# Kernel tuning notes

Hardware: AMD Instinct MI355X
Metric: run time of the kernel (lower is better)

## Reference

```python
import jax, jax.numpy as jnp
import numpy as np

N_FFT = 512; HOP = 256; WIN = 512
FDRC = 0.5; ORDER = 5; SPKS = 2
NFREQ = N_FFT // 2 + 1           # 257
HID = 512
PROJ = 2 * ORDER * SPKS * NFREQ  # 5140
LN_EPS = 1e-5
_WINDOW = 0.5 - 0.5 * jnp.cos(2 * jnp.pi * jnp.arange(WIN) / WIN)  # periodic hann


def _stft(x):
    # x: [B, L] -> complex spec [B, F, T], center-padded (reflect), hann window
    pad = N_FFT // 2
    xp = jnp.pad(x, ((0, 0), (pad, pad)), mode='reflect')
    T = 1 + (xp.shape[1] - N_FFT) // HOP
    idx = jnp.arange(T)[:, None] * HOP + jnp.arange(N_FFT)[None, :]
    frames = xp[:, idx] * _WINDOW            # [B, T, n_fft]
    spec = jnp.fft.rfft(frames, axis=-1)     # [B, T, F]
    return spec.transpose(0, 2, 1)           # [B, F, T]


def _istft(spec, length):
    # spec: [B, F, T] complex -> waveform [B, length] via overlap-add with window-square norm
    pad = N_FFT // 2
    frames = jnp.fft.irfft(spec.transpose(0, 2, 1), n=N_FFT, axis=-1) * _WINDOW  # [B,T,n_fft]
    B, T, _ = frames.shape
    total = length + 2 * pad
    idx = (jnp.arange(T)[:, None] * HOP + jnp.arange(N_FFT)[None, :]).ravel()
    out = jnp.zeros((B, total), frames.dtype).at[:, idx].add(frames.reshape(B, -1))
    wsq = jnp.zeros((total,), frames.dtype).at[idx].add(jnp.tile(_WINDOW ** 2, T))
    seg = wsq[pad:pad + length]
    return out[:, pad:pad + length] / jnp.where(seg > 1e-11, seg, 1.0)


def _lstm(xs, W_ih, W_hh, b_ih, b_hh):
    # xs: [T, B, in]; torch gate order i,f,g,o; returns hidden sequence [T, B, H]
    T, B, _ = xs.shape
    H = W_hh.shape[1]
    xs_proj = xs @ W_ih.T + (b_ih + b_hh)    # hoist input projection out of scan

    def step(carry, xp_t):
        h, c = carry
        gates = xp_t + h @ W_hh.T
        i, f, g, o = jnp.split(gates, 4, axis=-1)
        c = jax.nn.sigmoid(f) * c + jax.nn.sigmoid(i) * jnp.tanh(g)
        h = jax.nn.sigmoid(o) * jnp.tanh(c)
        return (h, c), h

    init = (jnp.zeros((B, H), xs.dtype), jnp.zeros((B, H), xs.dtype))
    _, hs = jax.lax.scan(step, init, xs_proj)
    return hs


def setup_inputs() -> dict:
    key = jax.random.key(0)
    ks = jax.random.split(key, 14)
    s = 0.04  # ~ 1/sqrt(hidden)
    return {
        'x': jax.random.normal(ks[0], (32, 160000), dtype=jnp.float32),
        'ln_g': jnp.ones((NFREQ,), jnp.float32),
        'ln_b': jnp.zeros((NFREQ,), jnp.float32),
        'W_ih0': jax.random.normal(ks[1], (4 * HID, NFREQ), jnp.float32) * s,
        'W_hh0': jax.random.normal(ks[2], (4 * HID, HID), jnp.float32) * s,
        'b_ih0': jax.random.normal(ks[3], (4 * HID,), jnp.float32) * s,
        'b_hh0': jax.random.normal(ks[4], (4 * HID,), jnp.float32) * s,
        'W_ih1': jax.random.normal(ks[5], (4 * HID, HID), jnp.float32) * s,
        'W_hh1': jax.random.normal(ks[6], (4 * HID, HID), jnp.float32) * s,
        'b_ih1': jax.random.normal(ks[7], (4 * HID,), jnp.float32) * s,
        'b_hh1': jax.random.normal(ks[8], (4 * HID,), jnp.float32) * s,
        'proj_W': jax.random.normal(ks[9], (PROJ, HID), jnp.float32) * s,
        'proj_b': jax.random.normal(ks[10], (PROJ,), jnp.float32) * s,
    }


def reference(x, ln_g, ln_b, W_ih0, W_hh0, b_ih0, b_hh0,
              W_ih1, W_hh1, b_ih1, b_hh1, proj_W, proj_b):
    B, L = x.shape
    spec = _stft(x)                      # [B, F, T] complex
    T = spec.shape[-1]
    mag = jnp.abs(spec) ** FDRC          # [B, F, T]

    # full-band sequence model (pre-LN -> 2-layer LSTM -> proj -> tanh)
    h = mag.transpose(2, 0, 1)           # [T, B, F]
    mu = h.mean(-1, keepdims=True)
    var = h.var(-1, keepdims=True)
    h = (h - mu) / jnp.sqrt(var + LN_EPS) * ln_g + ln_b
    h = _lstm(h, W_ih0, W_hh0, b_ih0, b_hh0)
    h = _lstm(h, W_ih1, W_hh1, b_ih1, b_hh1)
    h = jnp.tanh(h @ proj_W.T + proj_b)  # [T, B, 2*d*s*F]
    fb = h.transpose(1, 2, 0)            # [B, 2*d*s*F, T]

    # deep-filter coefficients: 'b (c d s f) t -> b d s f t c' -> complex [B,d,s,F,T]
    coef = fb.reshape(B, 2, ORDER, SPKS, NFREQ, T)
    coef_c = jax.lax.complex(coef[:, 0], coef[:, 1])

    # unfold spectrogram along time with left pad of (order-1): [B, F, T, d]
    padded = jnp.pad(spec, ((0, 0), (0, 0), (ORDER - 1, 0)))
    spec_unf = jnp.stack([padded[:, :, d:d + T] for d in range(ORDER)], axis=-1)

    # out[b,s,f,t] = sum_d spec_unf[b,f,t,d] * coef[b,d,s,f,t]
    enh = jnp.einsum('bftd,bdsft->bsft', spec_unf, coef_c)  # [B, S, F, T]

    enh_y = _istft(enh.reshape(B * SPKS, NFREQ, T), L).reshape(B, SPKS, L)
    return enh_y
```

## Files before the change

### kernel.cpp

```cpp
#include <hip/hip_runtime.h>
#include <hip/hip_cooperative_groups.h>
#include <math.h>

#define BATCH 32
#define LEN   160000
#define NFFT  512
#define NT    626
#define NF    257
#define NFP   288
#define HID   512
#define PROJN 5140
#define TC    32
#define NCHUNK 20
#define K0    800
#define K1    1024
#define NLSTM 64
#define NWORK 192
#define NBLKT 256

typedef unsigned short ushort;
typedef __attribute__((ext_vector_type(8))) short short8;
typedef __attribute__((ext_vector_type(4))) float f32x4;

__device__ __forceinline__ float sigm(float x){ return 1.0f/(1.0f+expf(-x)); }
__device__ __forceinline__ ushort f2bf(float f){
  union{float f;unsigned u;} v; v.f=f;
  unsigned r = v.u + 0x7fffu + ((v.u>>16)&1u);
  return (ushort)(r>>16);
}

__global__ __launch_bounds__(256) void k_init(float* tw, int* zr, int nz){
  int i = blockIdx.x*256 + threadIdx.x;
  if (i < 512){
    float ang = 6.28318530717958647692f * (float)i / 512.0f;
    tw[i]     = cosf(ang);
    tw[512+i] = sinf(ang);
  }
  for (int j = i; j < nz; j += gridDim.x*256) zr[j] = 0;
}

__global__ __launch_bounds__(256) void k_zero(float* p, int n){
  for (int i = blockIdx.x*256 + threadIdx.x; i < n; i += gridDim.x*256) p[i] = 0.f;
}

__global__ __launch_bounds__(256) void k_prep(const float* __restrict__ Wih0, const float* __restrict__ Whh0,
                                              const float* __restrict__ bih0, const float* __restrict__ bhh0,
                                              const float* __restrict__ Wih1, const float* __restrict__ Whh1,
                                              const float* __restrict__ bih1, const float* __restrict__ bhh1,
                                              const float* __restrict__ projW,
                                              ushort* __restrict__ W0, ushort* __restrict__ W1,
                                              float* __restrict__ b0c, float* __restrict__ b1c,
                                              ushort* __restrict__ projWb){
  const int n0 = 2048*K0, n1 = 2048*K1, n2 = PROJN*HID;
  for (int i = blockIdx.x*256 + threadIdx.x; i < n0 + n1 + 4096 + n2; i += gridDim.x*256){
    if (i < n0){
      int r = i / K0, c = i - r*K0;
      float v = (c < 257) ? Wih0[(size_t)r*257 + c] : (c < NFP ? 0.f : Whh0[(size_t)r*512 + (c-NFP)]);
      W0[i] = f2bf(v);
    } else if (i < n0 + n1){
      int j = i - n0;
      int r = j / K1, c = j - r*K1;
      float v = (c < 512) ? Wih1[(size_t)r*512 + c] : Whh1[(size_t)r*512 + (c-512)];
      W1[j] = f2bf(v);
    } else if (i < n0 + n1 + 4096){
      int j = i - n0 - n1;
      if (j < 2048) b0c[j] = bih0[j] + bhh0[j];
      else          b1c[j-2048] = bih1[j-2048] + bhh1[j-2048];
    } else {
      int j = i - n0 - n1 - 4096;
      projWb[j] = f2bf(projW[j]);
    }
  }
}

__global__ __launch_bounds__(256) void k_stftln(const float* __restrict__ x, const float* __restrict__ tw,
                                                const float* __restrict__ g, const float* __restrict__ be,
                                                ushort* __restrict__ hlnb){
  int b = blockIdx.x / NT;
  int t = blockIdx.x % NT;
  __shared__ float fr[NFFT], mg[NF];
  __shared__ float red[16];
  const float* xb = x + (size_t)b*LEN;
  for (int n = threadIdx.x; n < NFFT; n += 256){
    int j = t*256 + n - 256;
    if (j < 0) j = -j;
    else if (j >= LEN) j = 2*LEN - 2 - j;
    fr[n] = xb[j] * (0.5f - 0.5f*tw[n]);
  }
  __syncthreads();
  float v=0.f, v2=0.f;
  for (int f = threadIdx.x; f < NF; f += 256){
    float c4 = tw[(4*f)&511], s4 = tw[512+((4*f)&511)];
    float cr0=1.f,            si0=0.f;
    float cr1=tw[f&511],      si1=tw[512+(f&511)];
    float cr2=tw[(2*f)&511],  si2=tw[512+((2*f)&511)];
    float cr3=tw[(3*f)&511],  si3=tw[512+((3*f)&511)];
    float ar0=0.f,ai0=0.f,ar1=0.f,ai1=0.f,ar2=0.f,ai2=0.f,ar3=0.f,ai3=0.f;
    #pragma unroll 4
    for (int n = 0; n < NFFT; n += 4){
      ar0 += fr[n  ]*cr0; ai0 -= fr[n  ]*si0;
      ar1 += fr[n+1]*cr1; ai1 -= fr[n+1]*si1;
      ar2 += fr[n+2]*cr2; ai2 -= fr[n+2]*si2;
      ar3 += fr[n+3]*cr3; ai3 -= fr[n+3]*si3;
      float tc, ts;
      tc = cr0*c4 - si0*s4; ts = cr0*s4 + si0*c4; cr0=tc; si0=ts;
      tc = cr1*c4 - si1*s4; ts = cr1*s4 + si1*c4; cr1=tc; si1=ts;
      tc = cr2*c4 - si2*s4; ts = cr2*s4 + si2*c4; cr2=tc; si2=ts;
      tc = cr3*c4 - si3*s4; ts = cr3*s4 + si3*c4; cr3=tc; si3=ts;
    }
    float ar = (ar0+ar1)+(ar2+ar3);
    float ai = (ai0+ai1)+(ai2+ai3);
    float m = sqrtf(sqrtf(ar*ar + ai*ai));
    mg[f]=m; v+=m; v2+=m*m;
  }
  for (int off=32; off; off>>=1){ v += __shfl_down(v,off); v2 += __shfl_down(v2,off); }
  int w = threadIdx.x >> 6;
  if ((threadIdx.x & 63)==0){ red[w]=v; red[8+w]=v2; }
  __syncthreads();
  if (threadIdx.x==0){
    float s  = red[0]+red[1]+red[2]+red[3];
    float s2 = red[8]+red[9]+red[10]+red[11];
    float mu = s/(float)NF;
    red[4]=mu;
    red[5]=rsqrtf(s2/(float)NF - mu*mu + 1e-5f);
  }
  __syncthreads();
  float mu=red[4], rs=red[5];
  size_t ob = ((size_t)t*BATCH + b)*NFP;
  for (int f=threadIdx.x; f<NFP; f+=256){
    float val = 0.f;
    if (f < NF) val = (mg[f]-mu)*rs*g[f] + be[f];
    hlnb[ob+f] = f2bf(val);
  }
}

__device__ void dev_stft_frame(const float* __restrict__ x, const float* __restrict__ tw,
                               float* __restrict__ spR, float* __restrict__ spI,
                               int tb0, int tt, int b, float* fr){
  int t = tb0 + tt;
  int tid = threadIdx.x;
  if (t < 0 || t >= NT){
    for (int f = tid; f < NF; f += 256){
      size_t o = ((size_t)b*NF + f)*36 + tt;
      spR[o]=0.f; spI[o]=0.f;
    }
    return;
  }
  const float* xb = x + (size_t)b*LEN;
  for (int n = tid; n < NFFT; n += 256){
    int j = t*256 + n - 256;
    if (j < 0) j = -j;
    else if (j >= LEN) j = 2*LEN - 2 - j;
    fr[n] = xb[j] * (0.5f - 0.5f*tw[n]);
  }
  __syncthreads();
  for (int f = tid; f < NF; f += 256){
    float c4 = tw[(4*f)&511], s4 = tw[512+((4*f)&511)];
    float cr0=1.f,            si0=0.f;
    float cr1=tw[f&511],      si1=tw[512+(f&511)];
    float cr2=tw[(2*f)&511],  si2=tw[512+((2*f)&511)];
    float cr3=tw[(3*f)&511],  si3=tw[512+((3*f)&511)];
    float ar0=0.f,ai0=0.f,ar1=0.f,ai1=0.f,ar2=0.f,ai2=0.f,ar3=0.f,ai3=0.f;
    #pragma unroll 4
    for (int n = 0; n < NFFT; n += 4){
      ar0 += fr[n  ]*cr0; ai0 -= fr[n  ]*si0;
      ar1 += fr[n+1]*cr1; ai1 -= fr[n+1]*si1;
      ar2 += fr[n+2]*cr2; ai2 -= fr[n+2]*si2;
      ar3 += fr[n+3]*cr3; ai3 -= fr[n+3]*si3;
      float tc, ts;
      tc = cr0*c4 - si0*s4; ts = cr0*s4 + si0*c4; cr0=tc; si0=ts;
      tc = cr1*c4 - si1*s4; ts = cr1*s4 + si1*c4; cr1=tc; si1=ts;
      tc = cr2*c4 - si2*s4; ts = cr2*s4 + si2*c4; cr2=tc; si2=ts;
      tc = cr3*c4 - si3*s4; ts = cr3*s4 + si3*c4; cr3=tc; si3=ts;
    }
    size_t o = ((size_t)b*NF + f)*36 + tt;
    spR[o] = (ar0+ar1)+(ar2+ar3);
    spI[o] = (ai0+ai1)+(ai2+ai3);
  }
  __syncthreads();
}

__device__ void dev_gemm_tile(const ushort* __restrict__ A, const ushort* __restrict__ Bb,
                              const float* __restrict__ bias, float* __restrict__ C,
                              int M, int N, int bx, int by){
  int bm = by*64, bn = bx*64;
  int wave = threadIdx.x >> 6, lane = threadIdx.x & 63;
  int wm = wave >> 1, wn = wave & 1;
  int col = lane & 15, kg = lane >> 4;
  f32x4 acc00={0.f,0.f,0.f,0.f}, acc01=acc00, acc10=acc00, acc11=acc00;
  const ushort* Ap = A + (size_t)(bm + wm*32)*512;
  int nr0 = bn + wn*32 + col;
  int nr1 = nr0 + 16;
  const ushort* Bp0 = Bb + (size_t)((nr0<N)?nr0:0)*512;
  const ushort* Bp1 = Bb + (size_t)((nr1<N)?nr1:0)*512;
  #pragma unroll 4
  for (int k0=0; k0<512; k0+=32){
    short8 a0 = *(const short8*)(Ap + (size_t)col*512 + k0 + kg*8);
    short8 a1 = *(const short8*)(Ap + (size_t)(16+col)*512 + k0 + kg*8);
    short8 b0 = *(const short8*)(Bp0 + k0 + kg*8);
    short8 b1 = *(const short8*)(Bp1 + k0 + kg*8);
    acc00 = __builtin_amdgcn_mfma_f32_16x16x32_bf16(a0, b0, acc00, 0, 0, 0);
    acc01 = __builtin_amdgcn_mfma_f32_16x16x32_bf16(a0, b1, acc01, 0, 0, 0);
    acc10 = __builtin_amdgcn_mfma_f32_16x16x32_bf16(a1, b0, acc10, 0, 0, 0);
    acc11 = __builtin_amdgcn_mfma_f32_16x16x32_bf16(a1, b1, acc11, 0, 0, 0);
  }
  #define STORE_ACC(ACC, MI, NI) { \
    int n = bn + wn*32 + (NI)*16 + col; \
    if (n < N){ \
      float bv = bias[n]; \
      _Pragma("unroll") \
      for (int j=0;j<4;j++){ \
        int m = bm + wm*32 + (MI)*16 + kg*4 + j; \
        C[(size_t)m*N + n] = tanhf(ACC[j] + bv); \
      } \
    } }
  STORE_ACC(acc00, 0, 0)
  STORE_ACC(acc01, 0, 1)
  STORE_ACC(acc10, 1, 0)
  STORE_ACC(acc11, 1, 1)
  #undef STORE_ACC
}

__device__ void dev_ifused_task(const float* __restrict__ prch,
    const float* __restrict__ spR, const float* __restrict__ spI,
    const float* __restrict__ tw, float* __restrict__ out, int tb0, int task,
    float* reb, float* imb){
  int tl = task >> 6;
  int b  = (task >> 1) & 31;
  int s  = task & 1;
  int tau = tb0 + 4 + tl;
  int tid = threadIdx.x;
  const float* p = prch + ((size_t)tl*BATCH + b)*PROJN;
  for (int f=tid; f<NF; f+=256){
    float ar=0.f, ai=0.f;
    size_t so = ((size_t)b*NF + f)*36;
    #pragma unroll
    for (int d=0; d<5; d++){
      int ts = tb0 + tl + d;
      if (ts >= 0){
        float sr=spR[so + tl + d], si=spI[so + tl + d];
        float cr=p[d*514 + s*257 + f];
        float ci=p[2570 + d*514 + s*257 + f];
        ar += sr*cr - si*ci;
        ai += sr*ci + si*cr;
      }
    }
    reb[f]=ar; imb[f]=ai;
  }
  __syncthreads();
  float* ob = out + (size_t)(b*2+s)*LEN;
  for (int n=tid; n<NFFT; n+=256){
    float c4 = tw[(4*n)&511], s4 = tw[512+((4*n)&511)];
    float crA=tw[n&511],     siA=tw[512+(n&511)];
    float crB=tw[(2*n)&511], siB=tw[512+((2*n)&511)];
    float crC=tw[(3*n)&511], siC=tw[512+((3*n)&511)];
    float crD=c4,            siD=s4;
    float a0=0.f,a1=0.f,a2=0.f,a3=0.f;
    #pragma unroll 4
    for (int m=0; m<63; m++){
      int k = 4*m+1;
      a0 += reb[k  ]*crA - imb[k  ]*siA;
      a1 += reb[k+1]*crB - imb[k+1]*siB;
      a2 += reb[k+2]*crC - imb[k+2]*siC;
      a3 += reb[k+3]*crD - imb[k+3]*siD;
      float tc, ts;
      tc = crA*c4 - siA*s4; ts = crA*s4 + siA*c4; crA=tc; siA=ts;
      tc = crB*c4 - siB*s4; ts = crB*s4 + siB*c4; crB=tc; siB=ts;
      tc = crC*c4 - siC*s4; ts = crC*s4 + siC*c4; crC=tc; siC=ts;
      tc = crD*c4 - siD*s4; ts = crD*s4 + siD*c4; crD=tc; siD=ts;
    }
    a0 += reb[253]*crA - imb[253]*siA;
    a1 += reb[254]*crB - imb[254]*siB;
    a2 += reb[255]*crC - imb[255]*siC;
    float acc = reb[0] + ((n&1) ? -reb[256] : reb[256]) + 2.f*((a0+a1)+(a2+a3));
    int pos = tau*256 - 256 + n;
    if (pos >= 0 && pos < LEN)
      atomicAdd(ob + pos, acc * (1.0f/512.0f) * (0.5f - 0.5f*tw[n&511]));
  }
  __syncthreads();
}

__global__ __launch_bounds__(256, 1) void k_mega(const ushort* __restrict__ hlnb,
    const ushort* __restrict__ W0g, const ushort* __restrict__ W1g,
    const float* __restrict__ b0c, const float* __restrict__ b1c,
    ushort* __restrict__ h0b, ushort* __restrict__ h1b, ushort* __restrict__ h1hist,
    unsigned* __restrict__ flagsA, unsigned* __restrict__ epoch, unsigned* __restrict__ done,
    const float* __restrict__ x, const float* __restrict__ tw,
    const ushort* __restrict__ projWb, const float* __restrict__ projb,
    float* __restrict__ spR, float* __restrict__ spI, float* __restrict__ prch,
    float* __restrict__ out){
  __shared__ ushort Wlds0[32*808];
  __shared__ ushort Wlds1[32*1032];
  __shared__ float pc0[32][33];
  __shared__ float pc1[32][33];
  __shared__ float fr[NFFT];
  __shared__ float reb[NF], imb[NF];

  const int tid  = threadIdx.x;
  const int bid  = blockIdx.x;

  if (bid < NLSTM){
    const int u0   = bid << 3;
    const int wave = tid >> 6;
    const int lane = tid & 63;
    const int col  = lane & 15;
    const int kg   = lane >> 4;
    const int mh   = wave & 1;
    const int nh   = wave >> 1;
    const int arow = (mh<<4) + col;
    const int nlo  = (nh<<4) + col;

    for (int v = tid; v < 3200; v += 256){
      int r = v/100, c8 = v - r*100;
      int grow = ((r>>3)<<9) + u0 + (r&7);
      *(short8*)&Wlds0[r*808 + c8*8] = *(const short8*)(W0g + (size_t)grow*K0 + c8*8);
    }
    for (int v = tid; v < 4096; v += 256){
      int r = v>>7, c8 = v&127;
      int grow = ((r>>3)<<9) + u0 + (r&7);
      *(short8*)&Wlds1[r*1032 + c8*8] = *(const short8*)(W1g + (size_t)grow*K1 + c8*8);
    }
    const int bb = tid & 31;
    const int ul = tid >> 5;
    const int u  = u0 + ul;
    float bc0r[4], bc1r[4];
    #pragma unroll
    for (int g=0; g<4; g++){ bc0r[g] = b0c[(g<<9)+u]; bc1r[g] = b1c[(g<<9)+u]; }
    float c0r = 0.f, c1r = 0.f;
    const ushort* wb0 = &Wlds0[nlo*808];
    const ushort* wb1 = &Wlds1[nlo*1032];
    __syncthreads();

    f32x4 acc0x = {0.f,0.f,0.f,0.f};
    {
      const ushort* xt = hlnb;
      #pragma unroll
      for (int kt=0; kt<9; kt++){
        short8 a = *(const short8*)(xt + arow*NFP + kt*32 + kg*8);
        short8 b = *(const short8*)(wb0 + kt*32 + kg*8);
        acc0x = __builtin_amdgcn_mfma_f32_16x16x32_bf16(a, b, acc0x, 0, 0, 0);
      }
    }

    for (int t = 0; t <= NT; ++t){
      const ushort* h0p = h0b + (size_t)((t-1)&1)*(BATCH*HID);
      f32x4 acc0 = acc0x;
      f32x4 acc1 = {0.f,0.f,0.f,0.f};
      if (t >= 1){
        const ushort* h1p = h1b + (size_t)((t-2)&1)*(BATCH*HID);
        #pragma unroll
        for (int kt=0; kt<16; kt++){
          short8 a = *(const short8*)(h0p + arow*HID + kt*32 + kg*8);
          short8 b = *(const short8*)(wb1 + kt*32 + kg*8);
          acc1 = __builtin_amdgcn_mfma_f32_16x16x32_bf16(a, b, acc1, 0, 0, 0);
        }
        #pragma unroll
        for (int kt=0; kt<16; kt++){
          short8 a = *(const short8*)(h1p + arow*HID + kt*32 + kg*8);
          short8 b = *(const short8*)(wb1 + 512 + kt*32 + kg*8);
          acc1 = __builtin_amdgcn_mfma_f32_16x16x32_bf16(a, b, acc1, 0, 0, 0);
        }
      }
      if (t < NT){
        #pragma unroll
        for (int kt=0; kt<16; kt++){
          short8 a = *(const short8*)(h0p + arow*HID + kt*32 + kg*8);
          short8 b = *(const short8*)(wb0 + 288 + kt*32 + kg*8);
          acc0 = __builtin_amdgcn_mfma_f32_16x16x32_bf16(a, b, acc0, 0, 0, 0);
        }
      }
      if (t < NT){
        #pragma unroll
        for (int j=0;j<4;j++) pc0[(mh<<4)+(kg<<2)+j][nlo] = acc0[j];
      }
      if (t >= 1){
        #pragma unroll
        for (int j=0;j<4;j++) pc1[(mh<<4)+(kg<<2)+j][nlo] = acc1[j];
      }
      __syncthreads();
      if (t < NT){
        float p0 = pc0[bb][0*8+ul] + bc0r[0];
        float p1 = pc0[bb][1*8+ul] + bc0r[1];
        float p2 = pc0[bb][2*8+ul] + bc0r[2];
        float p3 = pc0[bb][3*8+ul] + bc0r[3];
        float cn = sigm(p1)*c0r + sigm(p0)*tanhf(p2);
        float hn = sigm(p3)*tanhf(cn);
        c0r = cn;
        h0b[(size_t)(t&1)*(BATCH*HID) + bb*HID + u] = f2bf(hn);
      }
      if (t >= 1){
        float p0 = pc1[bb][0*8+ul] + bc1r[0];
        float p1 = pc1[bb][1*8+ul] + bc1r[1];
        float p2 = pc1[bb][2*8+ul] + bc1r[2];
        float p3 = pc1[bb][3*8+ul] + bc1r[3];
        float cn = sigm(p1)*c1r + sigm(p0)*tanhf(p2);
        float hn = sigm(p3)*tanhf(cn);
        c1r = cn;
        ushort hb = f2bf(hn);
        h1b[(size_t)((t-1)&1)*(BATCH*HID) + bb*HID + u] = hb;
        __builtin_nontemporal_store(hb, h1hist + (size_t)t*(BATCH*HID) + bb*HID + u);
      }
      __syncthreads();
      if (tid == 0)
        __hip_atomic_store(&flagsA[bid*32], (unsigned)(t+1), __ATOMIC_RELEASE, __HIP_MEMORY_SCOPE_AGENT);
      acc0x = f32x4{0.f,0.f,0.f,0.f};
      if (t+1 < NT){
        const ushort* xt = hlnb + (size_t)(t+1)*BATCH*NFP;
        #pragma unroll
        for (int kt=0; kt<9; kt++){
          short8 a = *(const short8*)(xt + arow*NFP + kt*32 + kg*8);
          short8 b = *(const short8*)(wb0 + kt*32 + kg*8);
          acc0x = __builtin_amdgcn_mfma_f32_16x16x32_bf16(a, b, acc0x, 0, 0, 0);
        }
      }
      if (wave == 0){
        unsigned tgt = (unsigned)(t+1);
        while (true){
          unsigned v = __hip_atomic_load(&flagsA[lane*32], __ATOMIC_RELAXED, __HIP_MEMORY_SCOPE_AGENT);
          if (__all(v >= tgt)) break;
          __builtin_amdgcn_s_sleep(1);
        }
        if (bid == 0 && lane == 0)
          __hip_atomic_store(epoch, (unsigned)(t+1), __ATOMIC_RELAXED, __HIP_MEMORY_SCOPE_AGENT);
        (void)__hip_atomic_load(&flagsA[lane*32], __ATOMIC_ACQUIRE, __HIP_MEMORY_SCOPE_AGENT);
      }
      asm volatile("" ::: "memory");
      __syncthreads();
    }
    return;
  }

  const int w = bid - NLSTM;
  for (int c = 0; c < NCHUNK; ++c){
    int tcc = (c == NCHUNK-1) ? (NT - c*TC) : TC;
    int tb0 = c*TC - 4;
    unsigned need = (unsigned)(c*TC + tcc + 1);
    if (tid == 0){
      while (__hip_atomic_load(epoch, __ATOMIC_RELAXED, __HIP_MEMORY_SCOPE_AGENT) < need)
        __builtin_amdgcn_s_sleep(32);
      (void)__hip_atomic_load(epoch, __ATOMIC_ACQUIRE, __HIP_MEMORY_SCOPE_AGENT);
    }
    __syncthreads();
    for (int i = w; i < 36*BATCH; i += NWORK)
      dev_stft_frame(x, tw, spR, spI, tb0, i % 36, i / 36, fr);
    {
      unsigned* d0 = done + (c*3+0)*32;
      __syncthreads();
      if (tid == 0){
        __hip_atomic_fetch_add(d0, 1u, __ATOMIC_RELEASE, __HIP_MEMORY_SCOPE_AGENT);
        while (__hip_atomic_load(d0, __ATOMIC_RELAXED, __HIP_MEMORY_SCOPE_AGENT) < NWORK)
          __builtin_amdgcn_s_sleep(4);
        (void)__hip_atomic_load(d0, __ATOMIC_ACQUIRE, __HIP_MEMORY_SCOPE_AGENT);
      }
      __syncthreads();
    }
    {
      int gy = (tcc*BATCH)/64;
      int ntask = 81*gy;
      const ushort* A = h1hist + ((size_t)(c*TC)+1)*BATCH*HID;
      for (int i = w; i < ntask; i += NWORK)
        dev_gemm_tile(A, projWb, projb, prch, tcc*BATCH, PROJN, i % 81, i / 81);
      unsigned* d1 = done + (c*3+1)*32;
      __syncthreads();
      if (tid == 0){
        __hip_atomic_fetch_add(d1, 1u, __ATOMIC_RELEASE, __HIP_MEMORY_SCOPE_AGENT);
        while (__hip_atomic_load(d1, __ATOMIC_RELAXED, __HIP_MEMORY_SCOPE_AGENT) < NWORK)
          __builtin_amdgcn_s_sleep(4);
        (void)__hip_atomic_load(d1, __ATOMIC_ACQUIRE, __HIP_MEMORY_SCOPE_AGENT);
      }
      __syncthreads();
    }
    {
      for (int i = w; i < tcc*64; i += NWORK)
        dev_ifused_task(prch, spR, spI, tw, out, tb0, i, reb, imb);
      unsigned* d2 = done + (c*3+2)*32;
      __syncthreads();
      if (tid == 0){
        __hip_atomic_fetch_add(d2, 1u, __ATOMIC_RELEASE, __HIP_MEMORY_SCOPE_AGENT);
        while (__hip_atomic_load(d2, __ATOMIC_RELAXED, __HIP_MEMORY_SCOPE_AGENT) < NWORK)
          __builtin_amdgcn_s_sleep(4);
        (void)__hip_atomic_load(d2, __ATOMIC_ACQUIRE, __HIP_MEMORY_SCOPE_AGENT);
      }
      __syncthreads();
    }
  }
  for (size_t i = (size_t)w*256 + tid; i < (size_t)64*LEN; i += (size_t)NWORK*256){
    int m = (int)(i % LEN) & 255;
    float cm = tw[m];
    float w1 = 0.5f - 0.5f*cm;
    float w2 = 0.5f + 0.5f*cm;
    out[i] = out[i] / (w1*w1 + w2*w2);
  }
}

extern "C" void kernel_launch(void* const* d_in, const int* in_sizes, int n_in,
                              void* d_out, int out_size, void* d_ws, size_t ws_size,
                              hipStream_t stream){
  const float* x     = (const float*)d_in[0];
  const float* ln_g  = (const float*)d_in[1];
  const float* ln_b  = (const float*)d_in[2];
  const float* Wih0  = (const float*)d_in[3];
  const float* Whh0  = (const float*)d_in[4];
  const float* bih0  = (const float*)d_in[5];
  const float* bhh0  = (const float*)d_in[6];
  const float* Wih1  = (const float*)d_in[7];
  const float* Whh1  = (const float*)d_in[8];
  const float* bih1  = (const float*)d_in[9];
  const float* bhh1  = (const float*)d_in[10];
  const float* projW = (const float*)d_in[11];
  const float* projb = (const float*)d_in[12];

  char* base = (char*)d_ws;
  size_t off = 0;
  auto carve = [&](size_t bytes)->char*{
    char* p = base + off;
    off += (bytes + 255) & ~(size_t)255;
    return p;
  };
  float*  tw     = (float*) carve(1024*4);
  ushort* hlnb   = (ushort*)carve((size_t)NT*BATCH*NFP*2);
  ushort* W0     = (ushort*)carve((size_t)2048*K0*2);
  ushort* W1     = (ushort*)carve((size_t)2048*K1*2);
  float*  b0c    = (float*) carve(2048*4);
  float*  b1c    = (float*) carve(2048*4);
  ushort* projWb = (ushort*)carve((size_t)PROJN*HID*2);
  size_t zoff0 = off;
  ushort* h0b    = (ushort*)carve((size_t)2*BATCH*HID*2);
  ushort* h1b    = (ushort*)carve((size_t)2*BATCH*HID*2);
  unsigned* flagsA = (unsigned*)carve(NLSTM*32*4);
  unsigned* epoch  = (unsigned*)carve(128);
  unsigned* done   = (unsigned*)carve(NCHUNK*3*32*4);
  size_t zlen = off - zoff0;
  ushort* h1hist = (ushort*)carve((size_t)(NT+1)*BATCH*HID*2);
  float*  spR    = (float*) carve((size_t)BATCH*NF*36*4);
  float*  spI    = (float*) carve((size_t)BATCH*NF*36*4);
  float*  prch   = (float*) carve((size_t)TC*BATCH*PROJN*4);

  k_init<<<512, 256, 0, stream>>>(tw, (int*)(base + zoff0), (int)(zlen/4));
  k_zero<<<64, 256, 0, stream>>>((float*)h1hist, BATCH*HID/2);
  k_zero<<<2048, 256, 0, stream>>>((float*)d_out, out_size);
  k_prep<<<4096, 256, 0, stream>>>(Wih0, Whh0, bih0, bhh0, Wih1, Whh1, bih1, bhh1,
                                   projW, W0, W1, b0c, b1c, projWb);
  k_stftln<<<BATCH*NT, 256, 0, stream>>>(x, tw, ln_g, ln_b, hlnb);

  {
    float* outp = (float*)d_out;
    void* args[] = { (void*)&hlnb, (void*)&W0, (void*)&W1, (void*)&b0c, (void*)&b1c,
                     (void*)&h0b, (void*)&h1b, (void*)&h1hist,
                     (void*)&flagsA, (void*)&epoch, (void*)&done,
                     (void*)&x, (void*)&tw, (void*)&projWb, (void*)&projb,
                     (void*)&spR, (void*)&spI, (void*)&prch, (void*)&outp };
    hipLaunchCooperativeKernel(reinterpret_cast<void*>(k_mega), dim3(NBLKT), dim3(256),
                               args, 0, stream);
  }
}
```

Measured before the change: 9.266 ms.

## Fuse STFT+LayerNorm into mega kernel, overlapping it with the LSTM recurrence

Removes the separate STFT/LayerNorm launch and runs that work inside the cooperative mega kernel on the worker blocks. The work is split into 40 groups of time frames, and each group raises its own completion counter. LSTM blocks wait only for the group covering the upcoming timestep, so the spectrogram computation overlaps the sequential recurrence. Spin-wait sleep intervals on the worker barriers are also lengthened. The cost is extra polling in the LSTM critical loop and possible stalls if the STFT groups fall behind.

```diff
diff --git a/kernel.cpp b/kernel.cpp
--- a/kernel.cpp
+++ b/kernel.cpp
@@ -17,6 +17,7 @@
 #define NLSTM 64
 #define NWORK 192
 #define NBLKT 256
+#define NGRP  40
 
 typedef unsigned short ushort;
 typedef __attribute__((ext_vector_type(8))) short short8;
@@ -73,15 +74,13 @@
   }
 }
 
-__global__ __launch_bounds__(256) void k_stftln(const float* __restrict__ x, const float* __restrict__ tw,
-                                                const float* __restrict__ g, const float* __restrict__ be,
-                                                ushort* __restrict__ hlnb){
-  int b = blockIdx.x / NT;
-  int t = blockIdx.x % NT;
-  __shared__ float fr[NFFT], mg[NF];
-  __shared__ float red[16];
+__device__ void dev_stftln(const float* __restrict__ x, const float* __restrict__ tw,
+                           const float* __restrict__ g, const float* __restrict__ be,
+                           ushort* __restrict__ hlnb, int b, int t,
+                           float* fr, float* mg, float* red){
+  int tid = threadIdx.x;
   const float* xb = x + (size_t)b*LEN;
-  for (int n = threadIdx.x; n < NFFT; n += 256){
+  for (int n = tid; n < NFFT; n += 256){
     int j = t*256 + n - 256;
     if (j < 0) j = -j;
     else if (j >= LEN) j = 2*LEN - 2 - j;
@@ -89,7 +88,7 @@
   }
   __syncthreads();
   float v=0.f, v2=0.f;
-  for (int f = threadIdx.x; f < NF; f += 256){
+  for (int f = tid; f < NF; f += 256){
     float c4 = tw[(4*f)&511], s4 = tw[512+((4*f)&511)];
     float cr0=1.f,            si0=0.f;
     float cr1=tw[f&511],      si1=tw[512+(f&511)];
@@ -114,10 +113,10 @@
     mg[f]=m; v+=m; v2+=m*m;
   }
   for (int off=32; off; off>>=1){ v += __shfl_down(v,off); v2 += __shfl_down(v2,off); }
-  int w = threadIdx.x >> 6;
-  if ((threadIdx.x & 63)==0){ red[w]=v; red[8+w]=v2; }
-  __syncthreads();
-  if (threadIdx.x==0){
+  int w = tid >> 6;
+  if ((tid & 63)==0){ red[w]=v; red[8+w]=v2; }
+  __syncthreads();
+  if (tid==0){
     float s  = red[0]+red[1]+red[2]+red[3];
     float s2 = red[8]+red[9]+red[10]+red[11];
     float mu = s/(float)NF;
@@ -127,11 +126,12 @@
   __syncthreads();
   float mu=red[4], rs=red[5];
   size_t ob = ((size_t)t*BATCH + b)*NFP;
-  for (int f=threadIdx.x; f<NFP; f+=256){
+  for (int f=tid; f<NFP; f+=256){
     float val = 0.f;
     if (f < NF) val = (mg[f]-mu)*rs*g[f] + be[f];
     hlnb[ob+f] = f2bf(val);
   }
+  __syncthreads();
 }
 
 __device__ void dev_stft_frame(const float* __restrict__ x, const float* __restrict__ tw,
@@ -280,12 +280,14 @@
   __syncthreads();
 }
 
-__global__ __launch_bounds__(256, 1) void k_mega(const ushort* __restrict__ hlnb,
+__global__ __launch_bounds__(256, 1) void k_mega(ushort* __restrict__ hlnb,
     const ushort* __restrict__ W0g, const ushort* __restrict__ W1g,
     const float* __restrict__ b0c, const float* __restrict__ b1c,
     ushort* __restrict__ h0b, ushort* __restrict__ h1b, ushort* __restrict__ h1hist,
-    unsigned* __restrict__ flagsA, unsigned* __restrict__ epoch, unsigned* __restrict__ done,
+    unsigned* __restrict__ flagsA, unsigned* __restrict__ epoch,
+    unsigned* __restrict__ done, unsigned* __restrict__ gdone,
     const float* __restrict__ x, const float* __restrict__ tw,
+    const float* __restrict__ ln_g, const float* __restrict__ ln_b,
     const ushort* __restrict__ projWb, const float* __restrict__ projb,
     float* __restrict__ spR, float* __restrict__ spI, float* __restrict__ prch,
     float* __restrict__ out){
@@ -295,6 +297,7 @@
   __shared__ float pc1[32][33];
   __shared__ float fr[NFFT];
   __shared__ float reb[NF], imb[NF];
+  __shared__ float red[16];
 
   const int tid  = threadIdx.x;
   const int bid  = blockIdx.x;
@@ -330,6 +333,14 @@
     const ushort* wb0 = &Wlds0[nlo*808];
     const ushort* wb1 = &Wlds1[nlo*1032];
     __syncthreads();
+
+    if (tid == 0){
+      while (__hip_atomic_load(&gdone[0], __ATOMIC_RELAXED, __HIP_MEMORY_SCOPE_AGENT) < NWORK)
+        __builtin_amdgcn_s_sleep(8);
+      (void)__hip_atomic_load(&gdone[0], __ATOMIC_ACQUIRE, __HIP_MEMORY_SCOPE_AGENT);
+    }
+    __syncthreads();
+    int gseen = 0;
 
     f32x4 acc0x = {0.f,0.f,0.f,0.f};
     {
@@ -403,6 +414,17 @@
       __syncthreads();
       if (tid == 0)
         __hip_atomic_store(&flagsA[bid*32], (unsigned)(t+1), __ATOMIC_RELEASE, __HIP_MEMORY_SCOPE_AGENT);
+      if (wave == 0){
+        int greq = (t+5) >> 4; if (greq > NGRP-1) greq = NGRP-1;
+        if (greq > gseen){
+          if (lane == 0){
+            while (__hip_atomic_load(&gdone[greq*32], __ATOMIC_RELAXED, __HIP_MEMORY_SCOPE_AGENT) < NWORK)
+              __builtin_amdgcn_s_sleep(2);
+            (void)__hip_atomic_load(&gdone[greq*32], __ATOMIC_ACQUIRE, __HIP_MEMORY_SCOPE_AGENT);
+          }
+          gseen = greq;
+        }
+      }
       acc0x = f32x4{0.f,0.f,0.f,0.f};
       if (t+1 < NT){
         const ushort* xt = hlnb + (size_t)(t+1)*BATCH*NFP;
@@ -431,13 +453,24 @@
   }
 
   const int w = bid - NLSTM;
+  for (int g = 0; g < NGRP; ++g){
+    int i0 = g*512;
+    int i1 = i0 + 512; if (i1 > NT*BATCH) i1 = NT*BATCH;
+    for (int i = i0 + w; i < i1; i += NWORK){
+      int t = i >> 5, b = i & 31;
+      dev_stftln(x, tw, ln_g, ln_b, hlnb, b, t, fr, reb, red);
+    }
+    __syncthreads();
+    if (tid == 0)
+      __hip_atomic_fetch_add(&gdone[g*32], 1u, __ATOMIC_RELEASE, __HIP_MEMORY_SCOPE_AGENT);
+  }
   for (int c = 0; c < NCHUNK; ++c){
     int tcc = (c == NCHUNK-1) ? (NT - c*TC) : TC;
     int tb0 = c*TC - 4;
     unsigned need = (unsigned)(c*TC + tcc + 1);
     if (tid == 0){
       while (__hip_atomic_load(epoch, __ATOMIC_RELAXED, __HIP_MEMORY_SCOPE_AGENT) < need)
-        __builtin_amdgcn_s_sleep(32);
+        __builtin_amdgcn_s_sleep(64);
       (void)__hip_atomic_load(epoch, __ATOMIC_ACQUIRE, __HIP_MEMORY_SCOPE_AGENT);
     }
     __syncthreads();
@@ -449,7 +482,7 @@
       if (tid == 0){
         __hip_atomic_fetch_add(d0, 1u, __ATOMIC_RELEASE, __HIP_MEMORY_SCOPE_AGENT);
         while (__hip_atomic_load(d0, __ATOMIC_RELAXED, __HIP_MEMORY_SCOPE_AGENT) < NWORK)
-          __builtin_amdgcn_s_sleep(4);
+          __builtin_amdgcn_s_sleep(16);
         (void)__hip_atomic_load(d0, __ATOMIC_ACQUIRE, __HIP_MEMORY_SCOPE_AGENT);
       }
       __syncthreads();
@@ -465,7 +498,7 @@
       if (tid == 0){
         __hip_atomic_fetch_add(d1, 1u, __ATOMIC_RELEASE, __HIP_MEMORY_SCOPE_AGENT);
         while (__hip_atomic_load(d1, __ATOMIC_RELAXED, __HIP_MEMORY_SCOPE_AGENT) < NWORK)
-          __builtin_amdgcn_s_sleep(4);
+          __builtin_amdgcn_s_sleep(16);
         (void)__hip_atomic_load(d1, __ATOMIC_ACQUIRE, __HIP_MEMORY_SCOPE_AGENT);
       }
       __syncthreads();
@@ -478,7 +511,7 @@
       if (tid == 0){
         __hip_atomic_fetch_add(d2, 1u, __ATOMIC_RELEASE, __HIP_MEMORY_SCOPE_AGENT);
         while (__hip_atomic_load(d2, __ATOMIC_RELAXED, __HIP_MEMORY_SCOPE_AGENT) < NWORK)
-          __builtin_amdgcn_s_sleep(4);
+          __builtin_amdgcn_s_sleep(16);
         (void)__hip_atomic_load(d2, __ATOMIC_ACQUIRE, __HIP_MEMORY_SCOPE_AGENT);
       }
       __syncthreads();
@@ -530,6 +563,7 @@
   unsigned* flagsA = (unsigned*)carve(NLSTM*32*4);
   unsigned* epoch  = (unsigned*)carve(128);
   unsigned* done   = (unsigned*)carve(NCHUNK*3*32*4);
+  unsigned* gdone  = (unsigned*)carve(NGRP*32*4);
   size_t zlen = off - zoff0;
   ushort* h1hist = (ushort*)carve((size_t)(NT+1)*BATCH*HID*2);
   float*  spR    = (float*) carve((size_t)BATCH*NF*36*4);
@@ -541,14 +575,14 @@
   k_zero<<<2048, 256, 0, stream>>>((float*)d_out, out_size);
   k_prep<<<4096, 256, 0, stream>>>(Wih0, Whh0, bih0, bhh0, Wih1, Whh1, bih1, bhh1,
                                    projW, W0, W1, b0c, b1c, projWb);
-  k_stftln<<<BATCH*NT, 256, 0, stream>>>(x, tw, ln_g, ln_b, hlnb);
 
   {
     float* outp = (float*)d_out;
     void* args[] = { (void*)&hlnb, (void*)&W0, (void*)&W1, (void*)&b0c, (void*)&b1c,
                      (void*)&h0b, (void*)&h1b, (void*)&h1hist,
-                     (void*)&flagsA, (void*)&epoch, (void*)&done,
-                     (void*)&x, (void*)&tw, (void*)&projWb, (void*)&projb,
+                     (void*)&flagsA, (void*)&epoch, (void*)&done, (void*)&gdone,
+                     (void*)&x, (void*)&tw, (void*)&ln_g, (void*)&ln_b,
+                     (void*)&projWb, (void*)&projb,
                      (void*)&spR, (void*)&spI, (void*)&prch, (void*)&outp };
     hipLaunchCooperativeKernel(reinterpret_cast<void*>(k_mega), dim3(NBLKT), dim3(256),
                                args, 0, stream);
```

Measured after the change: 9.628 ms. 3.9% more time.
